# Kernel tuning notes

Measured on AMD Instinct MI355X. Metric: run time of the kernel, lower is better.

## Reference

```python
import jax, jax.numpy as jnp
import numpy as np


def conv1x1(x, w, bias):
    # x: [B,C,H,W], w: [O,C], bias: [O]
    return jnp.einsum('bchw,oc->bohw', x, w) + bias[None, :, None, None]


def setup_inputs() -> dict:
    key = jax.random.key(0)
    ks = jax.random.split(key, 12)
    B, Cin_half, H, W = 8, 128, 128, 128
    Cin, Cout = 256, 256
    s_in = 1.0 / np.sqrt(Cin)
    s_out = 1.0 / np.sqrt(Cout)
    return {
        'a': jax.random.normal(ks[0], (B, Cin_half, H, W), jnp.float32),
        'b': jax.random.normal(ks[1], (B, Cin_half, H, W), jnp.float32),
        'w1': jax.random.uniform(ks[2], (Cout, Cin), jnp.float32, -s_in, s_in),
        'b1': jax.random.uniform(ks[3], (Cout,), jnp.float32, -s_in, s_in),
        'w2': jax.random.uniform(ks[4], (Cout, Cout), jnp.float32, -s_out, s_out),
        'b2': jax.random.uniform(ks[5], (Cout,), jnp.float32, -s_out, s_out),
        'w3': jax.random.uniform(ks[6], (Cout, Cout), jnp.float32, -s_out, s_out),
        'b3': jax.random.uniform(ks[7], (Cout,), jnp.float32, -s_out, s_out),
        'w4': jax.random.uniform(ks[8], (Cout, Cout), jnp.float32, -s_out, s_out),
        'b4': jax.random.uniform(ks[9], (Cout,), jnp.float32, -s_out, s_out),
    }


def reference(a, b, w1, b1, w2, b2, w3, b3, w4, b4):
    z = jnp.concatenate([a, b], axis=1)            # [B, Cin, H, W]
    z = conv1x1(z, w1, b1)                          # [B, C, H, W]
    B, C, H, W = z.shape
    q = conv1x1(z, w2, b2).reshape(B, C, H * W)     # [B, C, N]
    k = conv1x1(z, w3, b3).reshape(B, C, H * W)
    v = conv1x1(z, w4, b4).reshape(B, C, H * W)
    qk = jnp.einsum('bcn,bdn->bcd', q, k)           # [B, C, C] (q @ k^T)
    attn = jax.nn.softmax(qk, axis=-1)
    out = jnp.einsum('bcd,bdn->bcn', attn, v)       # [B, C, N]
    return out.reshape(B, C, H, W)
```

## Files before the change

### kernel.cpp

```cpp
#include <hip/hip_runtime.h>

typedef float  f4v  __attribute__((ext_vector_type(4)));
typedef __bf16 bf8v __attribute__((ext_vector_type(8)));
typedef unsigned int u32x2 __attribute__((ext_vector_type(2)));
typedef unsigned int u32x4 __attribute__((ext_vector_type(4)));
typedef unsigned short u16;

#define MFMA(a,b,c) __builtin_amdgcn_mfma_f32_16x16x32_bf16((a),(b),(c),0,0,0)
#define HW_N 16384

__device__ __forceinline__ u16 bf_rne(float x){
  unsigned u = __float_as_uint(x);
  u += 0x7fffu + ((u >> 16) & 1u);
  return (u16)(u >> 16);
}

__global__ void k_weights(const float* __restrict__ w1, const float* __restrict__ b1,
                          const float* __restrict__ w2, const float* __restrict__ b2,
                          const float* __restrict__ w3, const float* __restrict__ b3,
                          const float* __restrict__ w4, const float* __restrict__ b4,
                          float* __restrict__ Wq, float* __restrict__ WkT,
                          float* __restrict__ Wv, float* __restrict__ bq,
                          float* __restrict__ bk, float* __restrict__ bv)
{
  const int blk = blockIdx.x, t = threadIdx.x;
  if (blk == 96){
    float aq = 0.f, ak = 0.f, av = 0.f;
    for (int j = 0; j < 256; ++j){
      const float bb = b1[j];
      aq += w2[t*256 + j] * bb;
      ak += w3[t*256 + j] * bb;
      av += w4[t*256 + j] * bb;
    }
    bq[t] = aq + b2[t];
    bk[t] = ak + b3[t];
    bv[t] = av + b4[t];
    return;
  }
  for (int i = 0; i < 8; ++i){
    const int e   = blk*2048 + i*256 + t;
    const int mat = e >> 16;
    const int c   = (e >> 8) & 255;
    const int col = e & 255;
    const float* wsrc = (mat == 0) ? w2 : ((mat == 1) ? w3 : w4);
    float acc = 0.f;
    for (int j = 0; j < 256; ++j) acc += wsrc[c*256 + j] * w1[j*256 + col];
    if      (mat == 0) Wq [c*256 + col] = acc;
    else if (mat == 1) WkT[col*256 + c] = acc;
    else               Wv [c*256 + col] = acc;
  }
}

__global__ __launch_bounds__(512, 2) void k_gram(
    const float* __restrict__ xa, const float* __restrict__ xb,
    float* __restrict__ Gpart, float* __restrict__ spart)
{
  __shared__ u16 hbuf[2][256*64];
  __shared__ u16 lbuf[2][256*64];
  const int blk = blockIdx.x;
  const int b = blk >> 5, half = (blk >> 4) & 1, chunk = blk & 15;
  const int t = threadIdx.x;
  const int lane = t & 63, w = t >> 6;
  const int wr = w >> 1, wc = w & 1;
  const int c4 = t & 15, crow = t >> 4;

  const float* rowp[8];
#pragma unroll
  for (int p = 0; p < 8; ++p){
    const int c = crow + 32*p;
    const float* base = (c < 128) ? (xa + (size_t)(b*128 + c) * HW_N)
                                  : (xb + (size_t)(b*128 + (c-128)) * HW_N);
    rowp[p] = base + c4*4;
  }

  float ssum[8];
#pragma unroll
  for (int p = 0; p < 8; ++p) ssum[p] = 0.f;

  const f4v vzero = {0.f, 0.f, 0.f, 0.f};
  f4v acc[4][4];
#pragma unroll
  for (int i = 0; i < 4; ++i)
#pragma unroll
    for (int j = 0; j < 4; ++j) acc[i][j] = vzero;

  f4v ld[8];
  auto issue = [&](int s){
    const int n0 = chunk*1024 + s*64;
#pragma unroll
    for (int p = 0; p < 8; ++p) ld[p] = *(const f4v*)(rowp[p] + n0);
  };
  auto wbuf = [&](int bi){
#pragma unroll
    for (int p = 0; p < 8; ++p){
      const int c = crow + 32*p;
      const f4v v = ld[p];
      ssum[p] += (v[0] + v[1]) + (v[2] + v[3]);
      u16 h[4], l[4];
#pragma unroll
      for (int i = 0; i < 4; ++i){
        const float x = v[i];
        const u16 hb = bf_rne(x);
        const float hf = __uint_as_float(((unsigned)hb) << 16);
        h[i] = hb; l[i] = bf_rne(x - hf);
      }
      u32x2 hp, lp;
      hp[0] = (unsigned)h[0] | ((unsigned)h[1] << 16);
      hp[1] = (unsigned)h[2] | ((unsigned)h[3] << 16);
      lp[0] = (unsigned)l[0] | ((unsigned)l[1] << 16);
      lp[1] = (unsigned)l[2] | ((unsigned)l[3] << 16);
      const int off = c*64 + (((c4 >> 1) ^ (c & 7)) * 8) + (c4 & 1) * 4;
      *(u32x2*)&hbuf[bi][off] = hp;
      *(u32x2*)&lbuf[bi][off] = lp;
    }
  };
  auto mstep = [&](int bi){
#pragma unroll
    for (int kk = 0; kk < 2; ++kk){
      bf8v ah[4], al[4], bh[4], bl[4];
#pragma unroll
      for (int f = 0; f < 4; ++f){
        const int so = kk*4 + (lane >> 4);
        const int r  = wr*64 + f*16 + (lane & 15);
        const int oa = r*64 + ((so ^ (r & 7)) * 8);
        ah[f] = *(const bf8v*)&hbuf[bi][oa];
        al[f] = *(const bf8v*)&lbuf[bi][oa];
        const int rc = 128*half + wc*64 + f*16 + (lane & 15);
        const int ob = rc*64 + ((so ^ (rc & 7)) * 8);
        bh[f] = *(const bf8v*)&hbuf[bi][ob];
        bl[f] = *(const bf8v*)&lbuf[bi][ob];
      }
#pragma unroll
      for (int i = 0; i < 4; ++i)
#pragma unroll
        for (int j = 0; j < 4; ++j){
          acc[i][j] = MFMA(ah[i], bh[j], acc[i][j]);
          acc[i][j] = MFMA(ah[i], bl[j], acc[i][j]);
          acc[i][j] = MFMA(al[i], bh[j], acc[i][j]);
        }
    }
  };

  issue(0); wbuf(0); __syncthreads();
  for (int s = 0; s < 16; ++s){
    const int cur = s & 1;
    if (s < 15) issue(s + 1);
    mstep(cur);
    if (s < 15) wbuf(cur ^ 1);
    __syncthreads();
  }

  float* gp = Gpart + (size_t)((b*2 + half)*16 + chunk) * 32768;
#pragma unroll
  for (int i = 0; i < 4; ++i)
#pragma unroll
    for (int j = 0; j < 4; ++j){
      const int row = wr*64 + i*16 + ((lane >> 4) << 2);
      const int col = wc*64 + j*16 + (lane & 15);
#pragma unroll
      for (int r2 = 0; r2 < 4; ++r2)
        gp[(row + r2)*128 + col] = acc[i][j][r2];
    }

  if (half == 0){
#pragma unroll
    for (int p = 0; p < 8; ++p){
      float v = ssum[p];
      v += __shfl_xor(v, 1);
      v += __shfl_xor(v, 2);
      v += __shfl_xor(v, 4);
      v += __shfl_xor(v, 8);
      if ((lane & 15) == 0)
        spart[(b*16 + chunk)*256 + (crow + 32*p)] = v;
    }
  }
}

__global__ void k_redg(const float* __restrict__ Gpart, float* __restrict__ G)
{
  for (int k = 0; k < 8; ++k){
    const int o = blockIdx.x*2048 + k*256 + threadIdx.x;
    const int b = o >> 16, r = (o >> 8) & 255, col = o & 255;
    const int half = col >> 7, cc = col & 127;
    const float* p = Gpart + (size_t)(b*2 + half)*524288 + (size_t)r*128 + cc;
    float s = 0.f;
#pragma unroll
    for (int ch = 0; ch < 16; ++ch) s += p[ch*32768];
    G[o] = s;
  }
}

__device__ __forceinline__ float block_red(float v, int ismax, volatile float* red, int t){
#pragma unroll
  for (int m = 32; m; m >>= 1){
    const float o = __shfl_xor(v, m);
    v = ismax ? fmaxf(v, o) : (v + o);
  }
  if ((t & 63) == 0) red[t >> 6] = v;
  __syncthreads();
  const float r01 = ismax ? fmaxf(red[0], red[1]) : (red[0] + red[1]);
  const float r23 = ismax ? fmaxf(red[2], red[3]) : (red[2] + red[3]);
  v = ismax ? fmaxf(r01, r23) : (r01 + r23);
  __syncthreads();
  return v;
}

__global__ __launch_bounds__(256, 2) void k_attn(
    const float* __restrict__ G, const float* __restrict__ spart,
    const float* __restrict__ Wq, const float* __restrict__ WkT,
    const float* __restrict__ Wv, const float* __restrict__ bq,
    const float* __restrict__ bk, const float* __restrict__ bv,
    u16* __restrict__ Mfrag, float* __restrict__ cb)
{
  __shared__ float s_lds[256];
  __shared__ float wq_lds[4][256];
  __shared__ float t1_lds[4][256];
  __shared__ float a_lds[4][256];
  __shared__ float red[4];
  const int blk = blockIdx.x;
  const int b = blk >> 6, r0 = (blk & 63) * 4;
  const int t = threadIdx.x;

  float sv = 0.f;
#pragma unroll
  for (int ch = 0; ch < 16; ++ch) sv += spart[(b*16 + ch)*256 + t];
  s_lds[t] = sv;
#pragma unroll
  for (int ri = 0; ri < 4; ++ri) wq_lds[ri][t] = Wq[(r0 + ri)*256 + t];
  __syncthreads();

  float t1[4] = {0,0,0,0}, pv[4] = {0,0,0,0};
  const float* gb = G + (size_t)b * 65536;
  for (int k = 0; k < 256; ++k){
    const float g  = gb[k*256 + t];
    const float sk = s_lds[k];
#pragma unroll
    for (int ri = 0; ri < 4; ++ri){
      const float wqv = wq_lds[ri][k];
      t1[ri] += wqv * g;
      pv[ri] += wqv * sk;
    }
  }
#pragma unroll
  for (int ri = 0; ri < 4; ++ri) t1_lds[ri][t] = t1[ri];
  __syncthreads();

  float qk[4] = {0,0,0,0}, rd = 0.f;
  for (int n = 0; n < 256; ++n){
    const float wkt = WkT[n*256 + t];
    rd += wkt * s_lds[n];
#pragma unroll
    for (int ri = 0; ri < 4; ++ri) qk[ri] += t1_lds[ri][n] * wkt;
  }
  const float bkv = bk[t];
#pragma unroll
  for (int ri = 0; ri < 4; ++ri){
    const float bqv = bq[r0 + ri];
    qk[ri] += pv[ri]*bkv + bqv*rd + 16384.f*bqv*bkv;
  }

  float areg[4];
#pragma unroll
  for (int ri = 0; ri < 4; ++ri){
    const float m = block_red(qk[ri], 1, red, t);
    const float e = __expf(qk[ri] - m);
    const float s = block_red(e, 0, red, t);
    areg[ri] = e / s;
    a_lds[ri][t] = areg[ri];
  }
  const float bvv = bv[t];
#pragma unroll
  for (int ri = 0; ri < 4; ++ri){
    const float c = block_red(areg[ri]*bvv, 0, red, t);
    if (t == 0) cb[b*256 + r0 + ri] = c;
  }
  __syncthreads();

  float m4[4] = {0,0,0,0};
  for (int d = 0; d < 256; ++d){
    const float wv = Wv[d*256 + t];
#pragma unroll
    for (int ri = 0; ri < 4; ++ri) m4[ri] += a_lds[ri][d] * wv;
  }
  const int ks = t >> 5, lhi = (t >> 3) & 3, j = t & 7;
#pragma unroll
  for (int ri = 0; ri < 4; ++ri){
    const int o = r0 + ri;
    Mfrag[(size_t)b*65536 +
          (size_t)((((o >> 4)*8 + ks)*64) + (o & 15) + (lhi << 4))*8 + j] = bf_rne(m4[ri]);
  }
}

__global__ __launch_bounds__(512, 2) void k_out(
    const float* __restrict__ xa, const float* __restrict__ xb,
    const u16* __restrict__ Mfrag, const float* __restrict__ cb,
    float* __restrict__ out)
{
  __shared__ u16 xt[2][64*256];
  const int blk = blockIdx.x;
  const int b = blk >> 6, nchunk = blk & 63;
  const int t = threadIdx.x;
  const int lane = t & 63, w = t >> 6;
  const int wr = w >> 1, wc = w & 1;
  const int c4 = t & 15, crow = t >> 4;

  u32x4 af[4][8];
  const u16* mb = Mfrag + (size_t)b * 65536;
#pragma unroll
  for (int f = 0; f < 4; ++f)
#pragma unroll
    for (int ks = 0; ks < 8; ++ks){
      const int obi = wr*4 + f;
      af[f][ks] = *(const u32x4*)(mb + (size_t)((obi*8 + ks)*64 + lane)*8);
    }
#pragma unroll
  for (int f = 0; f < 4; ++f)
#pragma unroll
    for (int ks = 0; ks < 8; ++ks)
      asm volatile("" : "+a"(af[f][ks]));

  f4v cb4[4];
#pragma unroll
  for (int f = 0; f < 4; ++f)
    cb4[f] = *(const f4v*)(cb + b*256 + wr*64 + f*16 + ((lane >> 4) << 2));

  const float* rowp[8];
#pragma unroll
  for (int p = 0; p < 8; ++p){
    const int c = crow + 32*p;
    const float* base = (p < 4) ? (xa + (size_t)(b*128 + c)*HW_N)
                                : (xb + (size_t)(b*128 + (c-128))*HW_N);
    rowp[p] = base + c4*4;
  }

  f4v ld[8];
  auto issue = [&](int s){
    const int n0 = nchunk*256 + s*64;
#pragma unroll
    for (int p = 0; p < 8; ++p) ld[p] = *(const f4v*)(rowp[p] + n0);
  };
  auto cvtwrite = [&](int bi){
#pragma unroll
    for (int p = 0; p < 8; ++p){
      const int c = crow + 32*p;
      const f4v v = ld[p];
#pragma unroll
      for (int i = 0; i < 4; ++i){
        const int n = c4*4 + i;
        xt[bi][n*256 + (((c >> 3) ^ (n & 7) ^ ((n >> 3) & 7))*8) + (c & 7)] = bf_rne(v[i]);
      }
    }
  };

  const f4v vzero = {0.f, 0.f, 0.f, 0.f};
  float* outp = out + (size_t)b*256*HW_N;

  issue(0);
  cvtwrite(0);
  __syncthreads();

  for (int s = 0; s < 4; ++s){
    const int cur = s & 1;
    if (s < 3) issue(s + 1);

    const int n0 = nchunk*256 + s*64;
    f4v acc[4][2];
#pragma unroll
    for (int f = 0; f < 4; ++f){ acc[f][0] = vzero; acc[f][1] = vzero; }

#pragma unroll
    for (int ks = 0; ks < 8; ++ks){
      bf8v bfr[2];
#pragma unroll
      for (int g = 0; g < 2; ++g){
        const int n  = wc*32 + g*16 + (lane & 15);
        const int so = ks*4 + (lane >> 4);
        bfr[g] = *(const bf8v*)&xt[cur][n*256 + ((so ^ (n & 7) ^ ((n >> 3) & 7))*8)];
      }
#pragma unroll
      for (int f = 0; f < 4; ++f){
        acc[f][0] = MFMA(__builtin_bit_cast(bf8v, af[f][ks]), bfr[0], acc[f][0]);
        acc[f][1] = MFMA(__builtin_bit_cast(bf8v, af[f][ks]), bfr[1], acc[f][1]);
      }
    }

#pragma unroll
    for (int f = 0; f < 4; ++f)
#pragma unroll
      for (int g = 0; g < 2; ++g){
        const int row = wr*64 + f*16 + ((lane >> 4) << 2);
        const int col = n0 + wc*32 + g*16 + (lane & 15);
#pragma unroll
        for (int r2 = 0; r2 < 4; ++r2)
          outp[(size_t)(row + r2)*HW_N + col] = acc[f][g][r2] + cb4[f][r2];
      }

    if (s < 3) cvtwrite(cur ^ 1);
    __syncthreads();
  }
}

extern "C" void kernel_launch(void* const* d_in, const int* in_sizes, int n_in,
                              void* d_out, int out_size, void* d_ws, size_t ws_size,
                              hipStream_t stream)
{
  const float* xa = (const float*)d_in[0];
  const float* xb = (const float*)d_in[1];
  const float* w1 = (const float*)d_in[2];
  const float* b1 = (const float*)d_in[3];
  const float* w2 = (const float*)d_in[4];
  const float* b2 = (const float*)d_in[5];
  const float* w3 = (const float*)d_in[6];
  const float* b3 = (const float*)d_in[7];
  const float* w4 = (const float*)d_in[8];
  const float* b4 = (const float*)d_in[9];
  float* out = (float*)d_out;
  char*  ws  = (char*)d_ws;

  float* Gpart = (float*)(ws + 0);
  float* G     = (float*)(ws + 33554432);
  float* spart = (float*)(ws + 35651584);
  float* Wq    = (float*)(ws + 35782656);
  float* WkT   = (float*)(ws + 36044800);
  float* Wv    = (float*)(ws + 36306944);
  float* bq    = (float*)(ws + 36569088);
  float* bk    = (float*)(ws + 36570112);
  float* bv    = (float*)(ws + 36571136);
  u16*   Mfrag = (u16*)  (ws + 36572160);
  float* cb    = (float*)(ws + 37620736);

  hipLaunchKernelGGL(k_weights, dim3(97),  dim3(256), 0, stream,
                     w1,b1,w2,b2,w3,b3,w4,b4, Wq,WkT,Wv,bq,bk,bv);
  hipLaunchKernelGGL(k_gram,    dim3(256), dim3(512), 0, stream, xa, xb, Gpart, spart);
  hipLaunchKernelGGL(k_redg,    dim3(256), dim3(256), 0, stream, Gpart, G);
  hipLaunchKernelGGL(k_attn,    dim3(512), dim3(256), 0, stream,
                     G, spart, Wq, WkT, Wv, bq, bk, bv, Mfrag, cb);
  hipLaunchKernelGGL(k_out,     dim3(512), dim3(512), 0, stream, xa, xb, Mfrag, cb, out);
}
```

Baseline: 258.0 us.

## Shrink k_out stage tile to 32 columns and raise occupancy to 4 blocks

Reworks the output GEMM kernel so each block stages 32 spatial columns per step instead of 64, across 8 steps instead of 4. Each wave now owns 32 output rows across all 32 columns, so it holds half as many A fragments. Each thread loads 4 contiguous float4 values from a single input row, and the LDS swizzle changes to XOR with n&15. The smaller LDS footprint and lower register count allow launch bounds of 4 blocks per CU, raising occupancy to hide memory latency. The cost is more loop iterations and barriers, and each thread's global reads now cover 64 contiguous bytes per row instead of the earlier coalescing pattern.

```diff
diff --git a/kernel.cpp b/kernel.cpp
--- a/kernel.cpp
+++ b/kernel.cpp
@@ -291,63 +291,55 @@
   }
 }
 
-__global__ __launch_bounds__(512, 2) void k_out(
+__global__ __launch_bounds__(512, 4) void k_out(
     const float* __restrict__ xa, const float* __restrict__ xb,
     const u16* __restrict__ Mfrag, const float* __restrict__ cb,
     float* __restrict__ out)
 {
-  __shared__ u16 xt[2][64*256];
+  __shared__ u16 xt[2][32*256];
   const int blk = blockIdx.x;
   const int b = blk >> 6, nchunk = blk & 63;
   const int t = threadIdx.x;
   const int lane = t & 63, w = t >> 6;
-  const int wr = w >> 1, wc = w & 1;
-  const int c4 = t & 15, crow = t >> 4;
-
-  u32x4 af[4][8];
+  const int cr = t >> 1;
+  const int hf = t & 1;
+
+  u32x4 af[2][8];
   const u16* mb = Mfrag + (size_t)b * 65536;
 #pragma unroll
-  for (int f = 0; f < 4; ++f)
-#pragma unroll
-    for (int ks = 0; ks < 8; ++ks){
-      const int obi = wr*4 + f;
-      af[f][ks] = *(const u32x4*)(mb + (size_t)((obi*8 + ks)*64 + lane)*8);
-    }
-#pragma unroll
-  for (int f = 0; f < 4; ++f)
+  for (int f = 0; f < 2; ++f)
+#pragma unroll
+    for (int ks = 0; ks < 8; ++ks)
+      af[f][ks] = *(const u32x4*)(mb + (size_t)((((w*2 + f)*8 + ks)*64 + lane))*8);
+#pragma unroll
+  for (int f = 0; f < 2; ++f)
 #pragma unroll
     for (int ks = 0; ks < 8; ++ks)
       asm volatile("" : "+a"(af[f][ks]));
 
-  f4v cb4[4];
-#pragma unroll
-  for (int f = 0; f < 4; ++f)
-    cb4[f] = *(const f4v*)(cb + b*256 + wr*64 + f*16 + ((lane >> 4) << 2));
-
-  const float* rowp[8];
-#pragma unroll
-  for (int p = 0; p < 8; ++p){
-    const int c = crow + 32*p;
-    const float* base = (p < 4) ? (xa + (size_t)(b*128 + c)*HW_N)
-                                : (xb + (size_t)(b*128 + (c-128))*HW_N);
-    rowp[p] = base + c4*4;
-  }
-
-  f4v ld[8];
+  f4v cb4[2];
+#pragma unroll
+  for (int f = 0; f < 2; ++f)
+    cb4[f] = *(const f4v*)(cb + b*256 + w*32 + f*16 + ((lane >> 4) << 2));
+
+  const float* rowbase = (cr < 128) ? (xa + (size_t)(b*128 + cr)*HW_N)
+                                    : (xb + (size_t)(b*128 + (cr-128))*HW_N);
+  const float* rp = rowbase + hf*16;
+
+  f4v ld[4];
   auto issue = [&](int s){
-    const int n0 = nchunk*256 + s*64;
-#pragma unroll
-    for (int p = 0; p < 8; ++p) ld[p] = *(const f4v*)(rowp[p] + n0);
+    const int n0 = nchunk*256 + s*32;
+#pragma unroll
+    for (int q = 0; q < 4; ++q) ld[q] = *(const f4v*)(rp + n0 + q*4);
   };
   auto cvtwrite = [&](int bi){
 #pragma unroll
-    for (int p = 0; p < 8; ++p){
-      const int c = crow + 32*p;
-      const f4v v = ld[p];
+    for (int q = 0; q < 4; ++q){
+      const f4v v = ld[q];
 #pragma unroll
       for (int i = 0; i < 4; ++i){
-        const int n = c4*4 + i;
-        xt[bi][n*256 + (((c >> 3) ^ (n & 7) ^ ((n >> 3) & 7))*8) + (c & 7)] = bf_rne(v[i]);
+        const int n = hf*16 + q*4 + i;
+        xt[bi][n*256 + (((cr >> 3) ^ (n & 15))*8) + (cr & 7)] = bf_rne(v[i]);
       }
     }
   };
@@ -359,43 +351,43 @@
   cvtwrite(0);
   __syncthreads();
 
-  for (int s = 0; s < 4; ++s){
+  for (int s = 0; s < 8; ++s){
     const int cur = s & 1;
-    if (s < 3) issue(s + 1);
-
-    const int n0 = nchunk*256 + s*64;
-    f4v acc[4][2];
-#pragma unroll
-    for (int f = 0; f < 4; ++f){ acc[f][0] = vzero; acc[f][1] = vzero; }
+    if (s < 7) issue(s + 1);
+
+    const int n0 = nchunk*256 + s*32;
+    f4v acc[2][2];
+#pragma unroll
+    for (int f = 0; f < 2; ++f){ acc[f][0] = vzero; acc[f][1] = vzero; }
 
 #pragma unroll
     for (int ks = 0; ks < 8; ++ks){
       bf8v bfr[2];
 #pragma unroll
       for (int g = 0; g < 2; ++g){
-        const int n  = wc*32 + g*16 + (lane & 15);
+        const int n  = g*16 + (lane & 15);
         const int so = ks*4 + (lane >> 4);
-        bfr[g] = *(const bf8v*)&xt[cur][n*256 + ((so ^ (n & 7) ^ ((n >> 3) & 7))*8)];
-      }
-#pragma unroll
-      for (int f = 0; f < 4; ++f){
+        bfr[g] = *(const bf8v*)&xt[cur][n*256 + ((so ^ (n & 15))*8)];
+      }
+#pragma unroll
+      for (int f = 0; f < 2; ++f){
         acc[f][0] = MFMA(__builtin_bit_cast(bf8v, af[f][ks]), bfr[0], acc[f][0]);
         acc[f][1] = MFMA(__builtin_bit_cast(bf8v, af[f][ks]), bfr[1], acc[f][1]);
       }
     }
 
 #pragma unroll
-    for (int f = 0; f < 4; ++f)
+    for (int f = 0; f < 2; ++f)
 #pragma unroll
       for (int g = 0; g < 2; ++g){
-        const int row = wr*64 + f*16 + ((lane >> 4) << 2);
-        const int col = n0 + wc*32 + g*16 + (lane & 15);
+        const int row = w*32 + f*16 + ((lane >> 4) << 2);
+        const int col = n0 + g*16 + (lane & 15);
 #pragma unroll
         for (int r2 = 0; r2 < 4; ++r2)
           outp[(size_t)(row + r2)*HW_N + col] = acc[f][g][r2] + cb4[f][r2];
       }
 
-    if (s < 3) cvtwrite(cur ^ 1);
+    if (s < 7) cvtwrite(cur ^ 1);
     __syncthreads();
   }
 }
```

Measured after the change: 248.5 us. -3.7%, faster.
